# Optimization experiments

Measured on AMD Instinct MI355X. Metric: run time of the kernel, lower is better.

The kernel has to match this reference:

```python
import jax, jax.numpy as jnp
import numpy as np

NUM_HEADS = 16
HEAD_DIM = 64
HIDDEN = NUM_HEADS * HEAD_DIM  # 1024
B, S = 2, 2048


def setup_inputs() -> dict:
    key = jax.random.key(0)
    ks = jax.random.split(key, 6)
    return {
        "hidden_states": jax.random.normal(ks[0], (B, S, HIDDEN), dtype=jnp.float32),
        "lora_state": jax.random.normal(ks[1], (B, S, 3 * HIDDEN), dtype=jnp.float32) * 0.02,
        "w_attn": jax.random.normal(ks[2], (HIDDEN, 3 * HIDDEN), dtype=jnp.float32) * 0.02,
        "b_attn": jax.random.normal(ks[3], (3 * HIDDEN,), dtype=jnp.float32) * 0.02,
        "w_proj": jax.random.normal(ks[4], (HIDDEN, HIDDEN), dtype=jnp.float32) * 0.02,
        "b_proj": jax.random.normal(ks[5], (HIDDEN,), dtype=jnp.float32) * 0.02,
    }


def reference(hidden_states, lora_state, w_attn, b_attn, w_proj, b_proj):
    b, s, d = hidden_states.shape
    # c_attn (GPT2 Conv1D: x @ W + b) plus LoRA correction added pre-split
    qkv = hidden_states @ w_attn + b_attn + lora_state  # [B,S,3D]
    q, k, v = jnp.split(qkv, 3, axis=-1)

    def split_heads(t):  # [B,S,D] -> [B,H,S,hd]
        return t.reshape(b, s, NUM_HEADS, HEAD_DIM).transpose(0, 2, 1, 3)

    q, k, v = split_heads(q), split_heads(k), split_heads(v)

    # eager attention: full [B,H,S,S] scores (faithful to the original)
    attn_weights = jnp.einsum("bhqd,bhkd->bhqk", q, k)
    attn_weights = attn_weights / jnp.asarray(HEAD_DIM ** 0.5, attn_weights.dtype)
    # causal mask via where with finfo.min, as in the torch code
    causal = jnp.tril(jnp.ones((s, s), dtype=bool))
    mask_value = jnp.finfo(attn_weights.dtype).min
    attn_weights = jnp.where(causal[None, None], attn_weights, mask_value)
    attn_weights = jax.nn.softmax(attn_weights, axis=-1)
    # dropout is identity in eval mode
    attn_output = jnp.einsum("bhqk,bhkd->bhqd", attn_weights, v)

    # merge heads [B,H,S,hd] -> [B,S,D]
    attn_output = attn_output.transpose(0, 2, 1, 3).reshape(b, s, d)
    attn_output = attn_output @ w_proj + b_proj
    return attn_output
```

## Files before the change

### kernel.cpp

```cpp
#include <hip/hip_runtime.h>
#include <hip/hip_bf16.h>
#include <cstdint>
#include <cstddef>

typedef unsigned short u16;
typedef unsigned int u32;
using f32x4  = __attribute__((ext_vector_type(4))) float;
using bf16x8 = __attribute__((ext_vector_type(8))) short;

__device__ __forceinline__ u16 f2bf(float f) {
    u32 u = __builtin_bit_cast(u32, f);
    u32 r = u + 0x7fffu + ((u >> 16) & 1u);
    return (u16)(r >> 16);
}

__device__ __forceinline__ void gload16(const u16* g, u16* l) {
    __builtin_amdgcn_global_load_lds(
        (const __attribute__((address_space(1))) void*)g,
        (__attribute__((address_space(3))) void*)l,
        16, 0, 0);
}

__global__ void k_convert(const float* __restrict__ src, u16* __restrict__ dst, int n4) {
    int i = blockIdx.x * blockDim.x + threadIdx.x;
    int stride = gridDim.x * blockDim.x;
    for (; i < n4; i += stride) {
        float4 v = ((const float4*)src)[i];
        ushort4 o;
        o.x = f2bf(v.x); o.y = f2bf(v.y); o.z = f2bf(v.z); o.w = f2bf(v.w);
        ((ushort4*)dst)[i] = o;
    }
}

__global__ void k_tconv(const float* __restrict__ src, u16* __restrict__ dst, int K, int N) {
    __shared__ float tile[32][33];
    int nb = blockIdx.x * 32, kb = blockIdx.y * 32;
    int tx = threadIdx.x, ty = threadIdx.y;
    #pragma unroll
    for (int j = 0; j < 32; j += 8)
        tile[ty + j][tx] = src[(size_t)(kb + ty + j) * N + nb + tx];
    __syncthreads();
    #pragma unroll
    for (int j = 0; j < 32; j += 8)
        dst[(size_t)(nb + ty + j) * K + kb + tx] = f2bf(tile[tx][ty + j]);
}

__device__ __forceinline__ void gemm128_mainloop(const u16* __restrict__ A,
                                                 const u16* __restrict__ Bt,
                                                 int m0, int n0, f32x4 (&acc)[4][4]) {
    __shared__ __align__(16) u16 As[2][128][32];
    __shared__ __align__(16) u16 Bs[2][128][32];
    const int t = threadIdx.x;
    const int lane = t & 63, wave = t >> 6;
    const int wr = wave >> 1, wc = wave & 1;
    const int g = lane >> 4, lr = lane & 15;

    #pragma unroll
    for (int mi = 0; mi < 4; mi++)
        #pragma unroll
        for (int ni = 0; ni < 4; ni++)
            acc[mi][ni] = (f32x4){0.f, 0.f, 0.f, 0.f};

    const int q0 = wave * 128 + lane;
    const int q1 = q0 + 64;
    const int r0 = q0 >> 2, c0 = (q0 & 3) * 8;
    const int r1 = q1 >> 2, c1 = (q1 & 3) * 8;
    u16* lA0 = &As[0][0][0] + wave * 1024;
    u16* lA1 = &As[1][0][0] + wave * 1024;
    u16* lB0 = &Bs[0][0][0] + wave * 1024;
    u16* lB1 = &Bs[1][0][0] + wave * 1024;
    const u16* gA0 = A  + (size_t)(m0 + r0) * 1024 + c0;
    const u16* gA1 = A  + (size_t)(m0 + r1) * 1024 + c1;
    const u16* gB0 = Bt + (size_t)(n0 + r0) * 1024 + c0;
    const u16* gB1 = Bt + (size_t)(n0 + r1) * 1024 + c1;

    auto STAGE = [&](u16* la, u16* lb, int kt) {
        gload16(gA0 + kt, la);
        gload16(gA1 + kt, la + 512);
        gload16(gB0 + kt, lb);
        gload16(gB1 + kt, lb + 512);
    };
    auto COMPUTE = [&](const u16 (*Asb)[32], const u16 (*Bsb)[32]) {
        bf16x8 af[4], bfr[4];
        #pragma unroll
        for (int mi = 0; mi < 4; mi++)
            af[mi] = *(const bf16x8*)&Asb[wr * 64 + mi * 16 + lr][g * 8];
        #pragma unroll
        for (int ni = 0; ni < 4; ni++)
            bfr[ni] = *(const bf16x8*)&Bsb[wc * 64 + ni * 16 + lr][g * 8];
        #pragma unroll
        for (int mi = 0; mi < 4; mi++)
            #pragma unroll
            for (int ni = 0; ni < 4; ni++)
                acc[mi][ni] = __builtin_amdgcn_mfma_f32_16x16x32_bf16(af[mi], bfr[ni], acc[mi][ni], 0, 0, 0);
    };

    STAGE(lA0, lB0, 0);
    STAGE(lA1, lB1, 32);

    for (int kt = 0; kt < 1024; kt += 64) {
        asm volatile("s_waitcnt vmcnt(4)" ::: "memory");
        __builtin_amdgcn_s_barrier();
        COMPUTE(As[0], Bs[0]);
        __builtin_amdgcn_s_barrier();
        asm volatile("" ::: "memory");
        if (kt + 64 < 1024) {
            STAGE(lA0, lB0, kt + 64);
            asm volatile("s_waitcnt vmcnt(4)" ::: "memory");
        } else {
            asm volatile("s_waitcnt vmcnt(0)" ::: "memory");
        }
        __builtin_amdgcn_s_barrier();
        COMPUTE(As[1], Bs[1]);
        __builtin_amdgcn_s_barrier();
        asm volatile("" ::: "memory");
        if (kt + 96 < 1024)
            STAGE(lA1, lB1, kt + 96);
    }
}

__global__ __launch_bounds__(256) void k_gemm_qkv(const u16* __restrict__ Xb, const u16* __restrict__ Wab,
                                                  const float* __restrict__ lora, const float* __restrict__ b_attn,
                                                  u16* __restrict__ Qb, u16* __restrict__ Kb, u16* __restrict__ Vt) {
    f32x4 acc[4][4];
    const int m0 = blockIdx.y * 128, n0 = blockIdx.x * 128;
    gemm128_mainloop(Xb, Wab, m0, n0, acc);
    const int lane = threadIdx.x & 63, wave = threadIdx.x >> 6;
    const int wr = wave >> 1, wc = wave & 1, g = lane >> 4, lr = lane & 15;
    #pragma unroll
    for (int mi = 0; mi < 4; mi++)
        #pragma unroll
        for (int ni = 0; ni < 4; ni++)
            #pragma unroll
            for (int r = 0; r < 4; r++) {
                int m = m0 + wr * 64 + mi * 16 + g * 4 + r;
                int n = n0 + wc * 64 + ni * 16 + lr;
                float v = acc[mi][ni][r] + b_attn[n] + lora[(size_t)m * 3072 + n];
                int which = n >> 10, rem = n & 1023, h = rem >> 6, hd = rem & 63;
                int b = m >> 11, s = m & 2047;
                size_t idx = ((size_t)(b * 16 + h) * 2048 + s) * 64 + hd;
                if (which == 0)      Qb[idx] = f2bf(v * 0.125f);
                else if (which == 1) Kb[idx] = f2bf(v);
                else Vt[((size_t)(b * 16 + h) * 64 + hd) * 2048 + s] = f2bf(v);
            }
}

__device__ __forceinline__ void attn_tile(const u16 (*Ks)[72], const u16 (*Vs)[72], u16 (*Ps)[72],
                                          int g, int lr, int rowq , int k0, bool diag,
                                          bf16x8 qf0, bf16x8 qf1,
                                          f32x4 (&accO)[4], float (&m_run)[4], float (&l_run)[4]) {
    f32x4 sc[4];
    #pragma unroll
    for (int ni = 0; ni < 4; ni++) {
        bf16x8 kf0 = *(const bf16x8*)&Ks[ni * 16 + lr][g * 8];
        bf16x8 kf1 = *(const bf16x8*)&Ks[ni * 16 + lr][32 + g * 8];
        f32x4 z = {0.f, 0.f, 0.f, 0.f};
        z = __builtin_amdgcn_mfma_f32_16x16x32_bf16(qf0, kf0, z, 0, 0, 0);
        z = __builtin_amdgcn_mfma_f32_16x16x32_bf16(qf1, kf1, z, 0, 0, 0);
        sc[ni] = z;
    }
    if (diag) {
        #pragma unroll
        for (int ni = 0; ni < 4; ni++)
            #pragma unroll
            for (int r = 0; r < 4; r++)
                if (k0 + ni * 16 + lr > rowq + g * 4 + r) sc[ni][r] = -INFINITY;
    }
    #pragma unroll
    for (int r = 0; r < 4; r++) {
        float mx = fmaxf(fmaxf(sc[0][r], sc[1][r]), fmaxf(sc[2][r], sc[3][r]));
        #pragma unroll
        for (int d = 1; d < 16; d <<= 1) mx = fmaxf(mx, __shfl_xor(mx, d, 64));
        float mnew = fmaxf(m_run[r], mx);
        float fsc = __expf(m_run[r] - mnew);
        float ls = 0.f;
        #pragma unroll
        for (int ni = 0; ni < 4; ni++) {
            float p = __expf(sc[ni][r] - mnew);
            sc[ni][r] = p;
            ls += p;
        }
        #pragma unroll
        for (int d = 1; d < 16; d <<= 1) ls += __shfl_xor(ls, d, 64);
        #pragma unroll
        for (int di = 0; di < 4; di++) accO[di][r] *= fsc;
        m_run[r] = mnew;
        l_run[r] = l_run[r] * fsc + ls;
    }
    #pragma unroll
    for (int ni = 0; ni < 4; ni++)
        #pragma unroll
        for (int r = 0; r < 4; r++)
            Ps[g * 4 + r][ni * 16 + lr] = f2bf(sc[ni][r]);
    #pragma unroll
    for (int e = 0; e < 2; e++) {
        bf16x8 pa = *(const bf16x8*)&Ps[lr][e * 32 + g * 8];
        #pragma unroll
        for (int di = 0; di < 4; di++) {
            bf16x8 vb = *(const bf16x8*)&Vs[di * 16 + lr][e * 32 + g * 8];
            accO[di] = __builtin_amdgcn_mfma_f32_16x16x32_bf16(pa, vb, accO[di], 0, 0, 0);
        }
    }
}

__global__ __launch_bounds__(256) void k_attn(const u16* __restrict__ Qb, const u16* __restrict__ Kb,
                                              const u16* __restrict__ Vt, u16* __restrict__ Ao) {
    __shared__ __align__(16) u16 Ks[64][72];
    __shared__ __align__(16) u16 Vs[64][72];
    __shared__ __align__(16) u16 Ps[4][16][72];
    const int i = blockIdx.x, bh = blockIdx.y;
    const int qtA = i, qtB = 31 - i;
    const int t = threadIdx.x, wave = t >> 6, lane = t & 63;
    const int g = lane >> 4, lr = lane & 15;
    const size_t bhO = (size_t)bh * (2048 * 64);
    const int q0A = qtA * 64, q0B = qtB * 64;
    const int rowqA = q0A + wave * 16, rowqB = q0B + wave * 16;

    bf16x8 qfA0 = *(const bf16x8*)(Qb + bhO + (size_t)(rowqA + lr) * 64 + g * 8);
    bf16x8 qfA1 = *(const bf16x8*)(Qb + bhO + (size_t)(rowqA + lr) * 64 + 32 + g * 8);
    bf16x8 qfB0 = *(const bf16x8*)(Qb + bhO + (size_t)(rowqB + lr) * 64 + g * 8);
    bf16x8 qfB1 = *(const bf16x8*)(Qb + bhO + (size_t)(rowqB + lr) * 64 + 32 + g * 8);

    f32x4 accA[4], accB[4];
    float mA[4], lA[4], mB[4], lB[4];
    #pragma unroll
    for (int x = 0; x < 4; x++) {
        accA[x] = (f32x4){0.f,0.f,0.f,0.f}; accB[x] = (f32x4){0.f,0.f,0.f,0.f};
        mA[x] = -INFINITY; lA[x] = 0.f; mB[x] = -INFINITY; lB[x] = 0.f;
    }

    const int sr0 = t >> 3,         sj0 = t & 7;
    const int sr1 = (t + 256) >> 3, sj1 = (t + 256) & 7;
    const u16* gK0 = Kb + bhO + (size_t)sr0 * 64 + sj0 * 8;
    const u16* gK1 = Kb + bhO + (size_t)sr1 * 64 + sj1 * 8;
    const u16* gV0 = Vt + bhO + (size_t)sr0 * 2048 + sj0 * 8;
    const u16* gV1 = Vt + bhO + (size_t)sr1 * 2048 + sj1 * 8;

    uint4 pk0 = *(const uint4*)(gK0);
    uint4 pk1 = *(const uint4*)(gK1);
    uint4 pv0 = *(const uint4*)(gV0);
    uint4 pv1 = *(const uint4*)(gV1);

    for (int kt = 0; kt <= qtB; ++kt) {
        const int k0 = kt * 64;
        __syncthreads();
        *(uint4*)&Ks[sr0][sj0 * 8] = pk0;
        *(uint4*)&Ks[sr1][sj1 * 8] = pk1;
        *(uint4*)&Vs[sr0][sj0 * 8] = pv0;
        *(uint4*)&Vs[sr1][sj1 * 8] = pv1;
        __syncthreads();

        if (kt < qtB) {
            const size_t kn = (size_t)(k0 + 64);
            pk0 = *(const uint4*)(gK0 + kn * 64);
            pk1 = *(const uint4*)(gK1 + kn * 64);
            pv0 = *(const uint4*)(gV0 + kn);
            pv1 = *(const uint4*)(gV1 + kn);
        }

        if (kt <= qtA)
            attn_tile(Ks, Vs, Ps[wave], g, lr, rowqA, k0, kt == qtA, qfA0, qfA1, accA, mA, lA);
        attn_tile(Ks, Vs, Ps[wave], g, lr, rowqB, k0, kt == qtB, qfB0, qfB1, accB, mB, lB);
    }

    const int b = bh >> 4, h = bh & 15;
    #pragma unroll
    for (int di = 0; di < 4; di++)
        #pragma unroll
        for (int r = 0; r < 4; r++) {
            int sA = rowqA + g * 4 + r;
            int sB = rowqB + g * 4 + r;
            Ao[((size_t)(b * 2048 + sA)) * 1024 + h * 64 + di * 16 + lr] = f2bf(accA[di][r] / lA[r]);
            Ao[((size_t)(b * 2048 + sB)) * 1024 + h * 64 + di * 16 + lr] = f2bf(accB[di][r] / lB[r]);
        }
}

__global__ __launch_bounds__(256) void k_gemm_proj(const u16* __restrict__ Ao, const u16* __restrict__ Wpb,
                                                   const float* __restrict__ b_proj, float* __restrict__ out) {
    f32x4 acc[4][4];
    const int m0 = blockIdx.y * 128, n0 = blockIdx.x * 128;
    gemm128_mainloop(Ao, Wpb, m0, n0, acc);
    const int lane = threadIdx.x & 63, wave = threadIdx.x >> 6;
    const int wr = wave >> 1, wc = wave & 1, g = lane >> 4, lr = lane & 15;
    #pragma unroll
    for (int mi = 0; mi < 4; mi++)
        #pragma unroll
        for (int ni = 0; ni < 4; ni++)
            #pragma unroll
            for (int r = 0; r < 4; r++) {
                int m = m0 + wr * 64 + mi * 16 + g * 4 + r;
                int n = n0 + wc * 64 + ni * 16 + lr;
                out[(size_t)m * 1024 + n] = acc[mi][ni][r] + b_proj[n];
            }
}

extern "C" void kernel_launch(void* const* d_in, const int* in_sizes, int n_in,
                              void* d_out, int out_size, void* d_ws, size_t ws_size,
                              hipStream_t stream) {
    const float* hidden = (const float*)d_in[0];
    const float* lora   = (const float*)d_in[1];
    const float* w_attn = (const float*)d_in[2];
    const float* b_attn = (const float*)d_in[3];
    const float* w_proj = (const float*)d_in[4];
    const float* b_proj = (const float*)d_in[5];
    float* out = (float*)d_out;

    char* ws = (char*)d_ws;
    u16* Xb  = (u16*)(ws + 0x0);
    u16* Wab = (u16*)(ws + 0x800000);
    u16* Wpb = (u16*)(ws + 0xE00000);
    u16* Qb  = (u16*)(ws + 0x1000000);
    u16* Kb  = (u16*)(ws + 0x1800000);
    u16* Vt  = (u16*)(ws + 0x2000000);
    u16* Ao  = Xb;

    k_convert<<<1024, 256, 0, stream>>>(hidden, Xb, (2 * 2048 * 1024) / 4);
    k_tconv<<<dim3(96, 32), dim3(32, 8), 0, stream>>>(w_attn, Wab, 1024, 3072);
    k_tconv<<<dim3(32, 32), dim3(32, 8), 0, stream>>>(w_proj, Wpb, 1024, 1024);
    k_gemm_qkv<<<dim3(24, 32), 256, 0, stream>>>(Xb, Wab, lora, b_attn, Qb, Kb, Vt);
    k_attn<<<dim3(16, 32), 256, 0, stream>>>(Qb, Kb, Vt, Ao);
    k_gemm_proj<<<dim3(8, 32), 256, 0, stream>>>(Ao, Wpb, b_proj, out);
}
```

Baseline: 317.3 us.

## Pre-convert lora+bias to bf16 and remap GEMM tiles per XCD

Adds a separate kernel that folds b_attn into lora_state and stores the sum as bf16, so the QKV GEMM epilogue reads 2-byte values instead of two fp32 loads. Both GEMMs also remap block IDs so each XCD handles a contiguous 8-row-by-N tile group, aiming for better L2 reuse of A and B tiles. The extra kernel still reads all of lora in fp32 and writes 24MB of bf16, so total traffic may go up. Rounding lora+bias to bf16 before adding it to the accumulator adds a small precision loss.

New measurement: 306.1 us. 3.5% less time.

```diff
diff --git a/kernel.cpp b/kernel.cpp
--- a/kernel.cpp
+++ b/kernel.cpp
@@ -12,6 +12,10 @@
     u32 u = __builtin_bit_cast(u32, f);
     u32 r = u + 0x7fffu + ((u >> 16) & 1u);
     return (u16)(r >> 16);
+}
+__device__ __forceinline__ float bf2f(u16 b) {
+    u32 u = ((u32)b) << 16;
+    return __builtin_bit_cast(float, u);
 }
 
 __device__ __forceinline__ void gload16(const u16* g, u16* l) {
@@ -28,6 +32,20 @@
         float4 v = ((const float4*)src)[i];
         ushort4 o;
         o.x = f2bf(v.x); o.y = f2bf(v.y); o.z = f2bf(v.z); o.w = f2bf(v.w);
+        ((ushort4*)dst)[i] = o;
+    }
+}
+
+__global__ void k_lorab(const float* __restrict__ lora, const float* __restrict__ b_attn,
+                        u16* __restrict__ dst, int n4) {
+    int i = blockIdx.x * blockDim.x + threadIdx.x;
+    int stride = gridDim.x * blockDim.x;
+    for (; i < n4; i += stride) {
+        float4 v = ((const float4*)lora)[i];
+        float4 bz = ((const float4*)b_attn)[i % 768];
+        ushort4 o;
+        o.x = f2bf(v.x + bz.x); o.y = f2bf(v.y + bz.y);
+        o.z = f2bf(v.z + bz.z); o.w = f2bf(v.w + bz.w);
         ((ushort4*)dst)[i] = o;
     }
 }
@@ -120,10 +138,16 @@
 }
 
 __global__ __launch_bounds__(256) void k_gemm_qkv(const u16* __restrict__ Xb, const u16* __restrict__ Wab,
-                                                  const float* __restrict__ lora, const float* __restrict__ b_attn,
+                                                  const u16* __restrict__ loraB,
                                                   u16* __restrict__ Qb, u16* __restrict__ Kb, u16* __restrict__ Vt) {
+    const int bid = blockIdx.y * 24 + blockIdx.x;
+    const int xcd = bid & 7, k = bid >> 3;
+    const int xm = xcd & 3, xn = xcd >> 2;
+    const int mt = xm * 8 + (k & 7);
+    const int nt = xn * 12 + (k >> 3);
+    const int m0 = mt * 128, n0 = nt * 128;
+
     f32x4 acc[4][4];
-    const int m0 = blockIdx.y * 128, n0 = blockIdx.x * 128;
     gemm128_mainloop(Xb, Wab, m0, n0, acc);
     const int lane = threadIdx.x & 63, wave = threadIdx.x >> 6;
     const int wr = wave >> 1, wc = wave & 1, g = lane >> 4, lr = lane & 15;
@@ -135,7 +159,7 @@
             for (int r = 0; r < 4; r++) {
                 int m = m0 + wr * 64 + mi * 16 + g * 4 + r;
                 int n = n0 + wc * 64 + ni * 16 + lr;
-                float v = acc[mi][ni][r] + b_attn[n] + lora[(size_t)m * 3072 + n];
+                float v = acc[mi][ni][r] + bf2f(loraB[(size_t)m * 3072 + n]);
                 int which = n >> 10, rem = n & 1023, h = rem >> 6, hd = rem & 63;
                 int b = m >> 11, s = m & 2047;
                 size_t idx = ((size_t)(b * 16 + h) * 2048 + s) * 64 + hd;
@@ -277,8 +301,14 @@
 
 __global__ __launch_bounds__(256) void k_gemm_proj(const u16* __restrict__ Ao, const u16* __restrict__ Wpb,
                                                    const float* __restrict__ b_proj, float* __restrict__ out) {
+    const int bid = blockIdx.y * 8 + blockIdx.x;
+    const int xcd = bid & 7, k = bid >> 3;
+    const int xm = xcd & 3, xn = xcd >> 2;
+    const int mt = xm * 8 + (k & 7);
+    const int nt = xn * 4 + (k >> 3);
+    const int m0 = mt * 128, n0 = nt * 128;
+
     f32x4 acc[4][4];
-    const int m0 = blockIdx.y * 128, n0 = blockIdx.x * 128;
     gemm128_mainloop(Ao, Wpb, m0, n0, acc);
     const int lane = threadIdx.x & 63, wave = threadIdx.x >> 6;
     const int wr = wave >> 1, wc = wave & 1, g = lane >> 4, lr = lane & 15;
@@ -306,18 +336,20 @@
     float* out = (float*)d_out;
 
     char* ws = (char*)d_ws;
-    u16* Xb  = (u16*)(ws + 0x0);
-    u16* Wab = (u16*)(ws + 0x800000);
-    u16* Wpb = (u16*)(ws + 0xE00000);
-    u16* Qb  = (u16*)(ws + 0x1000000);
-    u16* Kb  = (u16*)(ws + 0x1800000);
-    u16* Vt  = (u16*)(ws + 0x2000000);
-    u16* Ao  = Xb;
+    u16* Xb   = (u16*)(ws + 0x0);
+    u16* Wab  = (u16*)(ws + 0x800000);
+    u16* Wpb  = (u16*)(ws + 0xE00000);
+    u16* Qb   = (u16*)(ws + 0x1000000);
+    u16* Kb   = (u16*)(ws + 0x1800000);
+    u16* Vt   = (u16*)(ws + 0x2000000);
+    u16* lorB = (u16*)(ws + 0x2800000);
+    u16* Ao   = Xb;
 
     k_convert<<<1024, 256, 0, stream>>>(hidden, Xb, (2 * 2048 * 1024) / 4);
+    k_lorab<<<2048, 256, 0, stream>>>(lora, b_attn, lorB, (4096 * 3072) / 4);
     k_tconv<<<dim3(96, 32), dim3(32, 8), 0, stream>>>(w_attn, Wab, 1024, 3072);
     k_tconv<<<dim3(32, 32), dim3(32, 8), 0, stream>>>(w_proj, Wpb, 1024, 1024);
-    k_gemm_qkv<<<dim3(24, 32), 256, 0, stream>>>(Xb, Wab, lora, b_attn, Qb, Kb, Vt);
+    k_gemm_qkv<<<dim3(24, 32), 256, 0, stream>>>(Xb, Wab, lorB, Qb, Kb, Vt);
     k_attn<<<dim3(16, 32), 256, 0, stream>>>(Qb, Kb, Vt, Ao);
     k_gemm_proj<<<dim3(8, 32), 256, 0, stream>>>(Ao, Wpb, b_proj, out);
 }
```
